# Optimization experiments

Hardware: AMD Instinct MI355X
Metric: run time of the kernel (lower is better)

The kernel has to match this reference:

```python
import jax, jax.numpy as jnp
import numpy as np
import math

N = 524288
F = 8
NUM = 128          # num clusters (init arg `num`)
THRESHOLD = 1e-4   # init arg `threshold`
MAX_ITERS = 5      # fixed upper bound replacing the data-dependent while loop
EPS = 1e-6         # torch pairwise_distance eps (added to the difference)


def setup_inputs() -> dict:
    key = jax.random.key(0)
    k1, k2 = jax.random.split(key)
    data = jax.random.uniform(k1, (N, F), dtype=jnp.float32)      # coords in [0,1]
    centers = jax.random.uniform(k2, (NUM, F), dtype=jnp.float32)
    return {"data": data, "centers": centers}


def _assign(data, centers, r):
    """Sequential per-center assignment, faithful to the torch inner for-loop
    (including the D_value[indices] = update_mask * D zeroing behavior)."""
    n = data.shape[0]
    labels0 = -jnp.ones((n,), dtype=jnp.int32)
    dval0 = jnp.full((n,), 1000.0, dtype=data.dtype)

    def step(carry, ic):
        labels, dval = carry
        i, c = ic
        # spatial radius gate on first two coords
        sp = jnp.linalg.norm(data[:, :2] - c[:2], axis=1)          # [n]
        in_r = sp <= r
        enough = jnp.sum(in_r) > 1                                  # current_sum > 1
        # torch pairwise_distance: ||x - y + eps||_2
        D = jnp.sqrt(jnp.sum((data - c + EPS) ** 2, axis=1))        # [n]
        active = in_r & enough
        upd = active & (D < dval)
        # D_value[indices] = update_mask * D  (non-updated in-radius points -> 0)
        dval = jnp.where(active, jnp.where(upd, D, jnp.zeros_like(D)), dval)
        labels = jnp.where(upd, i, labels)
        return (labels, dval), None

    (labels, dval), _ = jax.lax.scan(
        step, (labels0, dval0), (jnp.arange(NUM, dtype=jnp.int32), centers))
    return labels, dval


def reference(data, centers):
    n = data.shape[0]
    r = 0.005 * math.sqrt(n / NUM)
    ones = jnp.ones((n,), dtype=data.dtype)
    labels_init = -jnp.ones((n,), dtype=jnp.int32)

    def outer(carry, _):
        cen, labels, converged = carry
        new_labels, _d = _assign(data, cen, r)
        # per-cluster mean; route unassigned (-1) points to a dummy segment
        safe = jnp.where(new_labels < 0, NUM, new_labels)
        sums = jax.ops.segment_sum(data, safe, num_segments=NUM + 1)[:NUM]   # [NUM, F]
        cnts = jax.ops.segment_sum(ones, safe, num_segments=NUM + 1)[:NUM]   # [NUM]
        mean_c = sums / jnp.maximum(cnts, 1.0)[:, None]
        # empty clusters (mean -> nan in torch) keep their old center
        new_c = jnp.where((cnts > 0)[:, None], mean_c, cen)
        diff = jnp.linalg.norm(new_c - cen)
        # freeze state once converged (emulates the while-loop break)
        new_c = jnp.where(converged, cen, new_c)
        new_labels = jnp.where(converged, labels, new_labels)
        converged = converged | (diff < THRESHOLD)
        return (new_c, new_labels, converged), None

    (centers_f, labels_f, _), _ = jax.lax.scan(
        outer, (centers, labels_init, jnp.array(False)), None, length=MAX_ITERS)
    # original returns (clusters, centers); clusters is just data grouped by labels,
    # which is ragged -> return (labels, centers) as the dense equivalent.
    return labels_f, centers_f
```

## Files before the change

### kernel.cpp

```cpp
#include <hip/hip_runtime.h>

#define NPTS 524288
#define NUMC 128
#define FD   8
#define NBLK 2048
#define ITERS 5

#define CSZ   512
#define FCOL  516
#define SLOTF (FD * FCOL)
#define RING  3

static_assert(NPTS == NBLK * 256, "grid must tile N exactly");

#define WAITVM(N) asm volatile("s_waitcnt vmcnt(" #N ")" ::: "memory")

__global__ void k_init(const float* __restrict__ cin, float* __restrict__ cen,
                       int* __restrict__ flag, int* __restrict__ cnt_inr) {
    int t = blockIdx.x * 256 + threadIdx.x;
    if (t < NUMC * FD) cen[t] = cin[t];
    if (t < NUMC) cnt_inr[t] = 0;
    if (t == 0) *flag = 0;
}

__global__ void k_count(const float* __restrict__ data, const float* __restrict__ cen,
                        int* __restrict__ cnt_inr, const int* __restrict__ flag) {
    if (*flag) return;
    __shared__ float cx[NUMC], cy[NUMC];
    __shared__ int hist[NUMC];
    int tid = threadIdx.x;
    if (tid < NUMC) { cx[tid] = cen[tid * FD]; cy[tid] = cen[tid * FD + 1]; hist[tid] = 0; }
    __syncthreads();
    size_t j = (size_t)blockIdx.x * 256 + tid;
    float2 p = *(const float2*)(data + j * FD);
    int lane = tid & 63;
    for (int i = 0; i < NUMC; i++) {
        float dx = __fsub_rn(p.x, cx[i]);
        float dy = __fsub_rn(p.y, cy[i]);
        float s  = __fadd_rn(__fmul_rn(dx, dx), __fmul_rn(dy, dy));
        bool in  = (__fsqrt_rn(s) <= 0.32f);
        unsigned long long m = __ballot(in);
        if (lane == 0 && m) atomicAdd(&hist[i], __popcll(m));
    }
    __syncthreads();
    if (tid < NUMC && hist[tid]) atomicAdd(&cnt_inr[tid], hist[tid]);
}

__global__ void k_assign(const float* __restrict__ data, const float* __restrict__ cen,
                         const int* __restrict__ cnt_inr, int* __restrict__ labels,
                         int* __restrict__ blockhist, const int* __restrict__ flag) {
    if (*flag) return;
    __shared__ float C[NUMC * FD];
    __shared__ int enough[NUMC];
    __shared__ int hist[NUMC];
    int tid = threadIdx.x;
    for (int e = tid; e < NUMC * FD; e += 256) C[e] = cen[e];
    if (tid < NUMC) { enough[tid] = (cnt_inr[tid] > 1); hist[tid] = 0; }
    __syncthreads();
    size_t j = (size_t)blockIdx.x * 256 + tid;
    float4 a = *(const float4*)(data + j * FD);
    float4 b = *(const float4*)(data + j * FD + 4);
    float x[8] = {a.x, a.y, a.z, a.w, b.x, b.y, b.z, b.w};
    int lab = -1;
    float dval = 1000.0f;
    for (int i = 0; i < NUMC; i++) {
        const float* c = &C[i * FD];
        float dx = __fsub_rn(x[0], c[0]);
        float dy = __fsub_rn(x[1], c[1]);
        float s  = __fadd_rn(__fmul_rn(dx, dx), __fmul_rn(dy, dy));
        float sp = __fsqrt_rn(s);
        if (sp <= 0.32f && enough[i]) {
            float t0 = __fadd_rn(__fsub_rn(x[0], c[0]), 1e-6f);
            float ss = __fmul_rn(t0, t0);
            #pragma unroll
            for (int f = 1; f < 8; f++) {
                float tf = __fadd_rn(__fsub_rn(x[f], c[f]), 1e-6f);
                ss = __fadd_rn(ss, __fmul_rn(tf, tf));
            }
            float D = __fsqrt_rn(ss);
            if (D < dval) { dval = D; lab = i; }
            else break;
        }
    }
    labels[j] = lab;
    if (lab >= 0) atomicAdd(&hist[lab], 1);
    __syncthreads();
    if (tid < NUMC) blockhist[tid * NBLK + blockIdx.x] = hist[tid];
}

__global__ void k_scan(int* __restrict__ blockhist, int* __restrict__ ctot, const int* __restrict__ flag) {
    if (*flag) return;
    int c = blockIdx.x, tid = threadIdx.x;
    __shared__ int ts[256];
    int base = c * NBLK + tid * 8;
    int v[8], s = 0;
    #pragma unroll
    for (int u = 0; u < 8; u++) { v[u] = blockhist[base + u]; s += v[u]; }
    ts[tid] = s;
    __syncthreads();
    for (int off = 1; off < 256; off <<= 1) {
        int t = (tid >= off) ? ts[tid - off] : 0;
        __syncthreads();
        ts[tid] += t;
        __syncthreads();
    }
    int run = (tid == 0) ? 0 : ts[tid - 1];
    #pragma unroll
    for (int u = 0; u < 8; u++) { int t = v[u]; blockhist[base + u] = run; run += t; }
    if (tid == 255) ctot[c] = run;
}

__global__ void k_base(const int* __restrict__ ctot, int* __restrict__ cbase, const int* __restrict__ flag) {
    if (*flag) return;
    if (threadIdx.x == 0) {
        int r = 0;
        for (int c = 0; c < NUMC; c++) { cbase[c] = r; r += ctot[c]; }
        cbase[NUMC] = r;
    }
}

__global__ void k_scatter(const float* __restrict__ data, const int* __restrict__ labels,
                          const int* __restrict__ blockhist, const int* __restrict__ cbase,
                          float* __restrict__ sorted, const int* __restrict__ flag) {
    if (*flag) return;
    __shared__ int sl[256];
    int tid = threadIdx.x;
    int j = blockIdx.x * 256 + tid;
    sl[tid] = labels[j];
    __syncthreads();
    int c = sl[tid];
    if (c >= 0) {
        int rank = 0;
        for (int t = 0; t < tid; t++) rank += (sl[t] == c);
        int pos = cbase[c] + blockhist[c * NBLK + blockIdx.x] + rank;
        float4 a = *(const float4*)(data + (size_t)j * FD);
        float4 b = *(const float4*)(data + (size_t)j * FD + 4);
        sorted[(size_t)0 * NPTS + pos] = a.x;
        sorted[(size_t)1 * NPTS + pos] = a.y;
        sorted[(size_t)2 * NPTS + pos] = a.z;
        sorted[(size_t)3 * NPTS + pos] = a.w;
        sorted[(size_t)4 * NPTS + pos] = b.x;
        sorted[(size_t)5 * NPTS + pos] = b.y;
        sorted[(size_t)6 * NPTS + pos] = b.z;
        sorted[(size_t)7 * NPTS + pos] = b.w;
    }
}

__device__ __forceinline__ void stage_chunk(const float* __restrict__ srt, int baseA,
                                            int t, int slot, float* sbuf, int lane) {
    const float* g0 = srt + (size_t)baseA + (size_t)t * CSZ + lane * 4;
    float* l0 = sbuf + slot * SLOTF;
    #pragma unroll
    for (int f = 0; f < FD; f++) {
        __builtin_amdgcn_global_load_lds(
            (const __attribute__((address_space(1))) void*)(g0 + (size_t)f * NPTS),
            (__attribute__((address_space(3))) void*)(l0 + f * FCOL),
            16, 0, 0);
        __builtin_amdgcn_global_load_lds(
            (const __attribute__((address_space(1))) void*)(g0 + (size_t)f * NPTS + 256),
            (__attribute__((address_space(3))) void*)(l0 + f * FCOL + 256),
            16, 0, 0);
    }
}

#define ADD4(v) { acc = __fadd_rn(acc, (v).x); acc = __fadd_rn(acc, (v).y); \
                  acc = __fadd_rn(acc, (v).z); acc = __fadd_rn(acc, (v).w); }

__global__ void __launch_bounds__(64) k_sums(const float* __restrict__ sorted,
                       const int* __restrict__ cbase, const int* __restrict__ ctot,
                       float* __restrict__ sums, const int* __restrict__ flag) {
    if (*flag) return;
    __shared__ float sbuf[RING * SLOTF];
    int c = blockIdx.x;
    int lane = threadIdx.x;
    int m = ctot[c], base = cbase[c];
    float acc = 0.0f;
    const float* col = sorted + (size_t)lane * NPTS + base;

    int A = (4 - (base & 3)) & 3;
    if (A > m) A = m;
    if (lane < FD)
        for (int k = 0; k < A; k++) acc = __fadd_rn(acc, col[k]);

    int baseA = base + A;
    int nch = (m - A) / CSZ;

    int pre = nch < RING ? nch : RING;
    for (int t = 0; t < pre; t++) stage_chunk(sorted, baseA, t, t, sbuf, lane);

    int slot = 0;
    for (int t = 0; t < nch; t++) {
        if (t >= 1 && t + 2 < nch)
            stage_chunk(sorted, baseA, t + 2, slot == 0 ? 2 : slot - 1, sbuf, lane);
        int K = nch - 1 - t; if (K > 2) K = 2;
        switch (K) {
            case 0: WAITVM(0);  break;
            case 1: WAITVM(16); break;
            default: WAITVM(32); break;
        }
        if (lane < FD) {
            const float* lcol = sbuf + slot * SLOTF + lane * FCOL;
            const float4* lv = (const float4*)lcol;
            float4 q[32];
            #pragma unroll
            for (int d = 0; d < 32; d++) q[d] = lv[d];
            #pragma unroll 32
            for (int b = 0; b < 96; b++) {
                float4 v = q[b & 31];
                ADD4(v);
                q[b & 31] = lv[b + 32];
            }
            #pragma unroll
            for (int b = 96; b < 128; b++) { float4 v = q[b & 31]; ADD4(v); }
        }
        slot = (slot == RING - 1) ? 0 : slot + 1;
    }

    if (lane < FD) {
        int start = A + nch * CSZ;
        int rem = m - start;
        const float* tcol = col + start;
        int tv = rem >> 2;
        const float4* tvp = (const float4*)tcol;
        float4 tb[16];
        #pragma unroll
        for (int d = 0; d < 16; d++) if (d < tv) tb[d] = tvp[d];
        int u = 0;
        for (; u + 32 <= tv; u += 16) {
            #pragma unroll
            for (int d = 0; d < 16; d++) {
                float4 v = tb[d];
                ADD4(v);
                tb[d] = tvp[u + 16 + d];
            }
        }
        #pragma unroll
        for (int d = 0; d < 16; d++) {
            if (u + d < tv) {
                float4 v = tb[d];
                ADD4(v);
                if (u + 16 + d < tv) tb[d] = tvp[u + 16 + d];
            }
        }
        u += 16;
        #pragma unroll
        for (int d = 0; d < 16; d++) {
            if (u + d < tv) { float4 v = tb[d]; ADD4(v); }
        }
        for (int k = tv << 2; k < rem; k++) acc = __fadd_rn(acc, tcol[k]);
        sums[c * FD + lane] = acc;
    }
}

__global__ void k_update(float* __restrict__ cen, const float* __restrict__ sums,
                         const int* __restrict__ ctot, int* __restrict__ flag,
                         int* __restrict__ cnt_inr) {
    if (*flag) return;
    __shared__ float red[256];
    int tid = threadIdx.x;
    if (tid < NUMC) cnt_inr[tid] = 0;
    float sq = 0.0f;
    float newv[4];
    int   eidx[4];
    int ne = 0;
    for (int e = tid; e < NUMC * FD; e += 256) {
        int c = e >> 3;
        float oldv = cen[e];
        float cntf = (float)ctot[c];
        float mean = __fdiv_rn(sums[e], fmaxf(cntf, 1.0f));
        float nc = (cntf > 0.0f) ? mean : oldv;
        float d = __fsub_rn(nc, oldv);
        sq = __fadd_rn(sq, __fmul_rn(d, d));
        newv[ne] = nc; eidx[ne] = e; ne++;
    }
    red[tid] = sq;
    __syncthreads();
    for (int off = 128; off > 0; off >>= 1) {
        if (tid < off) red[tid] += red[tid + off];
        __syncthreads();
    }
    for (int u = 0; u < ne; u++) cen[eidx[u]] = newv[u];
    if (tid == 0) {
        float diff = __fsqrt_rn(red[0]);
        if (diff < 1e-4f) *flag = 1;
    }
}

__global__ void k_finish(float* __restrict__ out, const float* __restrict__ cen) {
    size_t i = (size_t)blockIdx.x * 256 + threadIdx.x;
    if (i < NPTS) {
        int v = ((const int*)out)[i];
        out[i] = (float)v;
    } else if (i < NPTS + NUMC * FD) {
        out[i] = cen[i - NPTS];
    }
}

extern "C" void kernel_launch(void* const* d_in, const int* in_sizes, int n_in,
                              void* d_out, int out_size, void* d_ws, size_t ws_size,
                              hipStream_t stream) {
    const float* data = (const float*)d_in[0];
    const float* cen0 = (const float*)d_in[1];
    float* out = (float*)d_out;
    char* ws = (char*)d_ws;

    float* wcen   = (float*)(ws + 0);
    int*   flag   = (int*)(ws + 4096);
    int*   cntinr = (int*)(ws + 8192);
    int*   ctot   = (int*)(ws + 8704);
    int*   cbase  = (int*)(ws + 9216);
    float* sums   = (float*)(ws + 10240);
    int*   bh     = (int*)(ws + 16384);
    float* sorted = (float*)(ws + 16384 + (size_t)NUMC * NBLK * 4);
    int*   labels = (int*)d_out;

    k_init<<<4, 256, 0, stream>>>(cen0, wcen, flag, cntinr);
    for (int it = 0; it < ITERS; ++it) {
        k_count  <<<NBLK, 256, 0, stream>>>(data, wcen, cntinr, flag);
        k_assign <<<NBLK, 256, 0, stream>>>(data, wcen, cntinr, labels, bh, flag);
        k_scan   <<<NUMC, 256, 0, stream>>>(bh, ctot, flag);
        k_base   <<<1, 64, 0, stream>>>(ctot, cbase, flag);
        k_scatter<<<NBLK, 256, 0, stream>>>(data, labels, bh, cbase, sorted, flag);
        k_sums   <<<NUMC, 64, 0, stream>>>(sorted, cbase, ctot, sums, flag);
        k_update <<<1, 256, 0, stream>>>(wcen, sums, ctot, flag, cntinr);
    }
    k_finish<<<(NPTS + NUMC * FD + 255) / 256, 256, 0, stream>>>(out, wcen);
}
```

Baseline: 2.262 ms.

## Fuse base prefix into scan via last-block atomic, prefetch next chunk in sums

Removes the separate single-thread k_base launch by having the last k_scan block (detected with an atomic counter and threadfence) compute the exclusive prefix of cluster totals in parallel. In k_sums the per-chunk LDS load of the first 32 float4 is software-pipelined: the next slot's head is loaded while the current chunk's tail is accumulated, with waitcnt moved accordingly. This saves five launches and some LDS latency, but adds a global atomic and fence per scan block.

```diff
diff --git a/kernel.cpp b/kernel.cpp
--- a/kernel.cpp
+++ b/kernel.cpp
@@ -16,11 +16,12 @@
 #define WAITVM(N) asm volatile("s_waitcnt vmcnt(" #N ")" ::: "memory")
 
 __global__ void k_init(const float* __restrict__ cin, float* __restrict__ cen,
-                       int* __restrict__ flag, int* __restrict__ cnt_inr) {
+                       int* __restrict__ flag, int* __restrict__ cnt_inr,
+                       int* __restrict__ done) {
     int t = blockIdx.x * 256 + threadIdx.x;
     if (t < NUMC * FD) cen[t] = cin[t];
     if (t < NUMC) cnt_inr[t] = 0;
-    if (t == 0) *flag = 0;
+    if (t == 0) { *flag = 0; *done = 0; }
 }
 
 __global__ void k_count(const float* __restrict__ data, const float* __restrict__ cen,
@@ -88,10 +89,13 @@
     if (tid < NUMC) blockhist[tid * NBLK + blockIdx.x] = hist[tid];
 }
 
-__global__ void k_scan(int* __restrict__ blockhist, int* __restrict__ ctot, const int* __restrict__ flag) {
+__global__ void k_scan(int* __restrict__ blockhist, int* __restrict__ ctot,
+                       int* __restrict__ cbase, int* __restrict__ done,
+                       const int* __restrict__ flag) {
     if (*flag) return;
     int c = blockIdx.x, tid = threadIdx.x;
     __shared__ int ts[256];
+    __shared__ int amLast;
     int base = c * NBLK + tid * 8;
     int v[8], s = 0;
     #pragma unroll
@@ -107,15 +111,26 @@
     int run = (tid == 0) ? 0 : ts[tid - 1];
     #pragma unroll
     for (int u = 0; u < 8; u++) { int t = v[u]; blockhist[base + u] = run; run += t; }
-    if (tid == 255) ctot[c] = run;
-}
-
-__global__ void k_base(const int* __restrict__ ctot, int* __restrict__ cbase, const int* __restrict__ flag) {
-    if (*flag) return;
-    if (threadIdx.x == 0) {
-        int r = 0;
-        for (int c = 0; c < NUMC; c++) { cbase[c] = r; r += ctot[c]; }
-        cbase[NUMC] = r;
+    if (tid == 255) {
+        ctot[c] = run;
+        __threadfence();
+        amLast = (atomicAdd(done, 1) == NUMC - 1);
+    }
+    __syncthreads();
+    if (amLast) {
+        __threadfence();
+        int val = (tid < NUMC) ? ctot[tid] : 0;
+        ts[tid] = val;
+        __syncthreads();
+        for (int off = 1; off < NUMC; off <<= 1) {
+            int t2 = (tid >= off) ? ts[tid - off] : 0;
+            __syncthreads();
+            ts[tid] += t2;
+            __syncthreads();
+        }
+        if (tid < NUMC) cbase[tid] = ts[tid] - val;
+        if (tid == NUMC - 1) cbase[NUMC] = ts[tid];
+        if (tid == 0) *done = 0;
     }
 }
 
@@ -188,32 +203,48 @@
     int pre = nch < RING ? nch : RING;
     for (int t = 0; t < pre; t++) stage_chunk(sorted, baseA, t, t, sbuf, lane);
 
+    float4 q[32];
+    if (nch > 0) {
+        if (nch >= 3) { WAITVM(32); } else if (nch == 2) { WAITVM(16); } else { WAITVM(0); }
+        if (lane < FD) {
+            const float4* lv0 = (const float4*)(sbuf + lane * FCOL);
+            #pragma unroll
+            for (int d = 0; d < 32; d++) q[d] = lv0[d];
+        }
+    }
+
     int slot = 0;
     for (int t = 0; t < nch; t++) {
         if (t >= 1 && t + 2 < nch)
             stage_chunk(sorted, baseA, t + 2, slot == 0 ? 2 : slot - 1, sbuf, lane);
-        int K = nch - 1 - t; if (K > 2) K = 2;
-        switch (K) {
-            case 0: WAITVM(0);  break;
-            case 1: WAITVM(16); break;
-            default: WAITVM(32); break;
-        }
+        const float4* lv = (const float4*)(sbuf + slot * SLOTF + lane * FCOL);
         if (lane < FD) {
-            const float* lcol = sbuf + slot * SLOTF + lane * FCOL;
-            const float4* lv = (const float4*)lcol;
-            float4 q[32];
-            #pragma unroll
-            for (int d = 0; d < 32; d++) q[d] = lv[d];
             #pragma unroll 32
             for (int b = 0; b < 96; b++) {
                 float4 v = q[b & 31];
                 ADD4(v);
                 q[b & 31] = lv[b + 32];
             }
-            #pragma unroll
-            for (int b = 96; b < 128; b++) { float4 v = q[b & 31]; ADD4(v); }
-        }
-        slot = (slot == RING - 1) ? 0 : slot + 1;
+        }
+        int nslot = (slot == RING - 1) ? 0 : slot + 1;
+        if (t + 1 < nch) {
+            if (t + 2 < nch) { WAITVM(16); } else { WAITVM(0); }
+            if (lane < FD) {
+                const float4* lvn = (const float4*)(sbuf + nslot * SLOTF + lane * FCOL);
+                #pragma unroll
+                for (int b = 96; b < 128; b++) {
+                    float4 v = q[b & 31];
+                    ADD4(v);
+                    q[b & 31] = lvn[b - 96];
+                }
+            }
+        } else {
+            if (lane < FD) {
+                #pragma unroll
+                for (int b = 96; b < 128; b++) { float4 v = q[b & 31]; ADD4(v); }
+            }
+        }
+        slot = nslot;
     }
 
     if (lane < FD) {
@@ -310,16 +341,16 @@
     int*   ctot   = (int*)(ws + 8704);
     int*   cbase  = (int*)(ws + 9216);
     float* sums   = (float*)(ws + 10240);
+    int*   done   = (int*)(ws + 14336);
     int*   bh     = (int*)(ws + 16384);
     float* sorted = (float*)(ws + 16384 + (size_t)NUMC * NBLK * 4);
     int*   labels = (int*)d_out;
 
-    k_init<<<4, 256, 0, stream>>>(cen0, wcen, flag, cntinr);
+    k_init<<<4, 256, 0, stream>>>(cen0, wcen, flag, cntinr, done);
     for (int it = 0; it < ITERS; ++it) {
         k_count  <<<NBLK, 256, 0, stream>>>(data, wcen, cntinr, flag);
         k_assign <<<NBLK, 256, 0, stream>>>(data, wcen, cntinr, labels, bh, flag);
-        k_scan   <<<NUMC, 256, 0, stream>>>(bh, ctot, flag);
-        k_base   <<<1, 64, 0, stream>>>(ctot, cbase, flag);
+        k_scan   <<<NUMC, 256, 0, stream>>>(bh, ctot, cbase, done, flag);
         k_scatter<<<NBLK, 256, 0, stream>>>(data, labels, bh, cbase, sorted, flag);
         k_sums   <<<NUMC, 64, 0, stream>>>(sorted, cbase, ctot, sums, flag);
         k_update <<<1, 256, 0, stream>>>(wcen, sums, ctot, flag, cntinr);
```

New measurement: 2.090 ms, median of 2. 1.08x faster.
